# Kernel tuning notes

Measured on AMD Instinct MI355X. Metric: run time of the kernel, lower is better.

## Reference

```python
import jax, jax.numpy as jnp
import numpy as np

# Geometry constants hardcoded in the torch module
B, H, W = 1, 256, 256
A, DC = 64, 1024            # n_views, det_count
NSAMP = 512                  # samples per ray for the line integral
DSRC, DDET, SPACING = 500.0, 500.0, 2.0
NPAD = 2048                  # fft padding (next pow2 >= 2*DC)
FEAT = 32


def _bilinear_image(img, px, py):
    """Bilinear sample img (B,H,W) at centered coords px,py (any shape). Zero outside."""
    b, hh, ww = img.shape
    cx = px + (ww - 1) / 2.0
    cy = py + (hh - 1) / 2.0
    x0 = jnp.floor(cx); y0 = jnp.floor(cy)
    fx = cx - x0; fy = cy - y0
    x0i = x0.astype(jnp.int32); y0i = y0.astype(jnp.int32)
    flat = img.reshape(b, -1)

    def gather(yi, xi):
        valid = (yi >= 0) & (yi < hh) & (xi >= 0) & (xi < ww)
        yc = jnp.clip(yi, 0, hh - 1); xc = jnp.clip(xi, 0, ww - 1)
        idx = (yc * ww + xc).reshape(-1)
        v = jnp.take(flat, idx, axis=1).reshape((b,) + yi.shape)
        return v * valid.astype(img.dtype)

    return (gather(y0i, x0i) * (1 - fx) * (1 - fy)
            + gather(y0i, x0i + 1) * fx * (1 - fy)
            + gather(y0i + 1, x0i) * (1 - fx) * fy
            + gather(y0i + 1, x0i + 1) * fx * fy)


def fan_forward(img, theta):
    """Ray-driven fan-beam forward projection. img (B,1,H,W) -> sino (B,A,DC)."""
    im = img[:, 0]
    c = jnp.cos(theta); s = jnp.sin(theta)
    src = DSRC * jnp.stack([c, s], -1)                    # (A,2) source positions
    e = jnp.stack([-s, c], -1)                            # detector axis
    u = (jnp.arange(DC) - (DC - 1) / 2.0) * SPACING       # detector offsets
    det = -DDET * jnp.stack([c, s], -1)[:, None, :] + u[None, :, None] * e[:, None, :]  # (A,DC,2)
    d = det - src[:, None, :]
    L = jnp.sqrt(jnp.sum(d * d, axis=-1))                 # (A,DC) ray lengths
    t = (jnp.arange(NSAMP, dtype=jnp.float32) + 0.5) / NSAMP
    pts = src[:, None, None, :] + t[None, None, :, None] * d[:, :, None, :]  # (A,DC,N,2)
    vals = _bilinear_image(im, pts[..., 0], pts[..., 1])  # (B,A,DC,N)
    return jnp.sum(vals, axis=-1) * (L / NSAMP)[None]


def filter_sinogram(sino):
    """Ram-Lak ramp filtering along the detector axis with zero-padding."""
    f = jnp.abs(jnp.fft.rfftfreq(NPAD)).astype(jnp.float32)  # cycles/sample
    sf = jnp.fft.rfft(sino, n=NPAD, axis=-1) * (2.0 * f)
    return jnp.fft.irfft(sf, n=NPAD, axis=-1)[..., :DC].astype(sino.dtype)


def fan_backprojection(sino, theta):
    """Pixel-driven fan-beam backprojection. sino (B,A,DC) -> (B,1,H,W)."""
    xs = jnp.arange(W, dtype=jnp.float32) - (W - 1) / 2.0
    ys = jnp.arange(H, dtype=jnp.float32) - (H - 1) / 2.0
    gx, gy = jnp.meshgrid(xs, ys)                         # (H,W)
    c = jnp.cos(theta)[:, None, None]; s = jnp.sin(theta)[:, None, None]
    xr = gx[None] * c + gy[None] * s                      # (A,H,W) rotated coords
    yr = -gx[None] * s + gy[None] * c
    denom = DSRC - xr
    uu = yr * (DSRC + DDET) / denom                       # detector coordinate
    wgt = (DSRC * DSRC) / (denom * denom)                 # fan-beam distance weight
    iu = uu / SPACING + (DC - 1) / 2.0
    i0 = jnp.floor(iu); fr = iu - i0
    i0i = i0.astype(jnp.int32)
    aidx = jnp.arange(A)[:, None, None]
    b = sino.shape[0]
    flat = sino.reshape(b, -1)

    def g(ii):
        valid = (ii >= 0) & (ii < DC)
        ic = jnp.clip(ii, 0, DC - 1)
        idx = (aidx * DC + ic).reshape(-1)
        v = jnp.take(flat, idx, axis=1).reshape((b, A, H, W))
        return v * valid.astype(sino.dtype)

    vals = g(i0i) * (1 - fr) + g(i0i + 1) * fr            # (B,A,H,W)
    bp = jnp.sum(vals * wgt[None], axis=1) * (jnp.pi / A)
    return bp[:, None]


def conv(x, w):
    return jax.lax.conv_general_dilated(x, w, (1, 1), 'SAME',
                                        dimension_numbers=('NCHW', 'OIHW', 'NCHW'))


def setup_inputs():
    key = jax.random.key(0)
    ks = jax.random.split(key, 8)
    x = jax.random.normal(ks[0], (B, 1, H, W), jnp.float32)
    theta = jnp.arange(A, dtype=jnp.float32) * (2.0 * np.pi / A)
    sinogram = jax.random.normal(ks[1], (B, A, DC), jnp.float32)

    def xav(k, shape):
        fan_in = shape[1] * 9; fan_out = shape[0] * 9
        return jax.random.normal(k, shape, jnp.float32) * np.sqrt(2.0 / (fan_in + fan_out)).astype(np.float32)

    return {
        'x': x, 'theta': theta, 'sinogram': sinogram,
        'lambda_step': jnp.float32(0.5), 'soft_thr': jnp.float32(0.01),
        'conv1_forward': xav(ks[2], (FEAT, 1, 3, 3)),
        'conv2_forward': xav(ks[3], (FEAT, FEAT, 3, 3)),
        'conv1_backward': xav(ks[4], (FEAT, FEAT, 3, 3)),
        'conv2_backward': xav(ks[5], (1, FEAT, 3, 3)),
    }


def reference(x, theta, sinogram, lambda_step, soft_thr,
              conv1_forward, conv2_forward, conv1_backward, conv2_backward):
    sino_pred = fan_forward(x, theta)
    filtered = filter_sinogram(sino_pred)
    X_fbp = fan_backprojection(filtered - sinogram, theta)
    x_input = x - lambda_step * X_fbp
    h = jax.nn.relu(conv(x_input, conv1_forward))
    x_forward = conv(h, conv2_forward)
    hs = jnp.sign(x_forward) * jax.nn.relu(jnp.abs(x_forward) - soft_thr)
    x_pred = conv(jax.nn.relu(conv(hs, conv1_backward)), conv2_backward)
    x_est = conv(jax.nn.relu(conv(x_forward, conv1_backward)), conv2_backward)
    symloss = x_est - x_input
    return (x_pred, symloss)
```

## Files before the change

kernel.cpp:

```cpp
#include <hip/hip_runtime.h>

#define DEV_INLINE __device__ __forceinline__

#define PI_F 3.14159265358979323846f

#define H_OFF     0
#define SINO_OFF  2048
#define DIFF_OFF  67584
#define XIN_OFF   133120
#define WF2F_OFF  198656
#define WF1B_OFF  207872
#define WF2B_OFF  212480
#define BUFA_OFF  217088
#define BUFB_OFF  2314240

typedef short bf16x8 __attribute__((ext_vector_type(8)));
typedef float f32x4 __attribute__((ext_vector_type(4)));

union FragI4 { int4 i4; bf16x8 v; };
union FragI  { int i[4]; bf16x8 v; };
union I4U    { int4 i4; int i[4]; };

DEV_INLINE unsigned rne1(float a) {
  unsigned u = __float_as_uint(a);
  return (u + 0x7FFFu + ((u >> 16) & 1u)) >> 16;
}
DEV_INLINE int pack_rne(float a, float b) {
  return (int)(rne1(a) | (rne1(b) << 16));
}

__global__ __launch_bounds__(256) void setup_kernel(
    const float* __restrict__ sino_in, const float* __restrict__ w2f,
    const float* __restrict__ w1b, const float* __restrict__ w2b,
    const float* __restrict__ img,
    float* __restrict__ h, float* __restrict__ diff,
    int* __restrict__ wf2f, int* __restrict__ wf1b, int* __restrict__ wf2b,
    float4* __restrict__ quadP, float* __restrict__ x_input) {
  const int b = blockIdx.x;
  const int tid = threadIdx.x;
  if (b < 64) {
    __shared__ float hp[8][32];
    const int cell = tid & 31;
    const int kq = tid >> 5;
    const int n = b * 32 + cell;
    float ssum = 0.0f;
    const float ang_scale = PI_F / 1024.0f;
    for (int k = kq * 128; k < kq * 128 + 128; ++k) {
      int m = (k * n) & 2047;
      ssum += (float)k * __cosf((float)m * ang_scale);
    }
    hp[kq][cell] = ssum;
    __syncthreads();
    if (tid < 32) {
      float S = 0.0f;
      #pragma unroll
      for (int q = 0; q < 8; ++q) S += hp[q][tid];
      int nn = b * 32 + tid;
      float sgn = (nn & 1) ? -1.0f : 1.0f;
      h[nn] = (S * (1.0f / 512.0f) + sgn) * (1.0f / 2048.0f);
    }
  } else if (b < 320) {
    int idx = (b - 64) * 256 + tid;
    diff[idx] = -sino_in[idx];
  } else if (b < 356) {
    const bool second = (b >= 338);
    int idx = (b - (second ? 338 : 320)) * 256 + tid;
    int d = idx & 3;
    int L = (idx >> 2) & 63;
    int jm = idx >> 8;
    int j = jm >> 1, mt = jm & 1;
    int co = mt * 16 + (L & 15);
    int ci0 = (L >> 4) * 8 + 2 * d;
    const float* w = second ? w1b : w2f;
    int v = pack_rne(w[co * 288 + ci0 * 9 + j], w[co * 288 + (ci0 + 1) * 9 + j]);
    (second ? wf1b : wf2f)[idx] = v;
  } else if (b < 617) {
    int idx = (b - 356) * 256 + tid;
    if (idx < 258 * 258) {
      int y = idx / 258;
      int x = idx - y * 258;
      float4 v;
      int ay = y - 1, bx = x - 1;
      bool y0ok = (ay >= 0 && ay < 256);
      bool y1ok = (ay + 1 >= 0 && ay + 1 < 256);
      bool x0ok = (bx >= 0 && bx < 256);
      bool x1ok = (bx + 1 >= 0 && bx + 1 < 256);
      v.x = (y0ok && x0ok) ? img[(ay << 8) + bx] : 0.0f;
      v.y = (y0ok && x1ok) ? img[(ay << 8) + bx + 1] : 0.0f;
      v.z = (y1ok && x0ok) ? img[((ay + 1) << 8) + bx] : 0.0f;
      v.w = (y1ok && x1ok) ? img[((ay + 1) << 8) + bx + 1] : 0.0f;
      quadP[idx] = v;
    }
  } else if (b < 873) {
    int idx = (b - 617) * 256 + tid;
    x_input[idx] = img[idx];
  } else {
    int d = tid & 3;
    int L = tid >> 2;
    int n = L & 15;
    int k0 = (L >> 4) * 8 + 2 * d;
    float lo = (n < 9) ? w2b[k0 * 9 + n] : 0.0f;
    float hi = (n < 9) ? w2b[(k0 + 1) * 9 + n] : 0.0f;
    wf2b[tid] = pack_rne(lo, hi);
  }
}

__global__ __launch_bounds__(256) void fwdproj(
    const float4* __restrict__ quadP, const float* __restrict__ theta,
    float* __restrict__ sino) {
  __shared__ float part[8][32];
  __shared__ float cs[2];
  const int tid = threadIdx.x;
  const int a = blockIdx.x >> 5;
  const int cell = tid & 31;
  const int chunk = tid >> 5;
  const int d = ((blockIdx.x & 31) << 5) + cell;
  if (tid == 0) {
    float th = theta[a];
    cs[0] = cosf(th);
    cs[1] = sinf(th);
  }
  __syncthreads();
  const float c = cs[0], s = cs[1];
  const float u = ((float)d - 511.5f) * 2.0f;
  const float dxv = -1000.0f * c - u * s;
  const float dyv = -1000.0f * s + u * c;
  const float L = sqrtf(1.0e6f + u * u);
  const float sx = fmaf(500.0f, c, 127.5f);
  const float sy = fmaf(500.0f, s, 127.5f);

  float tlo = 0.0f, thi = 1.0f;
  if (fabsf(dxv) > 1e-6f) {
    float inv = 1.0f / dxv;
    float a0 = (-1.0f - sx) * inv, a1 = (256.0f - sx) * inv;
    tlo = fmaxf(tlo, fminf(a0, a1));
    thi = fminf(thi, fmaxf(a0, a1));
  } else if (sx <= -1.0f || sx >= 256.0f) {
    thi = -1.0f;
  }
  if (fabsf(dyv) > 1e-6f) {
    float inv = 1.0f / dyv;
    float a0 = (-1.0f - sy) * inv, a1 = (256.0f - sy) * inv;
    tlo = fmaxf(tlo, fminf(a0, a1));
    thi = fminf(thi, fmaxf(a0, a1));
  } else if (sy <= -1.0f || sy >= 256.0f) {
    thi = -1.0f;
  }
  int imin = (int)ceilf(tlo * 512.0f - 0.5f) - 1;
  imin = imin < 0 ? 0 : imin;
  int imax = (int)floorf(thi * 512.0f - 0.5f) + 1;
  imax = imax > 511 ? 511 : imax;

  float acc = 0.0f;
  for (int i = imin + chunk; i <= imax; i += 8) {
    float t = ((float)i + 0.5f) * (1.0f / 512.0f);
    float cx = fmaf(t, dxv, sx);
    float cy = fmaf(t, dyv, sy);
    cx = fminf(fmaxf(cx, -1.0f), 256.0f);
    cy = fminf(fmaxf(cy, -1.0f), 256.0f);
    float xf = floorf(cx), yf = floorf(cy);
    float fx = cx - xf, fy = cy - yf;
    int ix = (int)xf + 1;
    int iy = (int)yf + 1;
    float4 q = quadP[iy * 258 + ix];
    float gx = 1.0f - fx, gy = 1.0f - fy;
    acc += gy * (gx * q.x + fx * q.y) + fy * (gx * q.z + fx * q.w);
  }
  part[chunk][cell] = acc;
  __syncthreads();
  if (tid < 32) {
    float r = 0.0f;
    #pragma unroll
    for (int q = 0; q < 8; ++q) r += part[q][tid];
    sino[a * 1024 + ((blockIdx.x & 31) << 5) + tid] = r * (L * (1.0f / 512.0f));
  }
}

__global__ __launch_bounds__(256) void filt(
    const float* __restrict__ sino_pred, const float* __restrict__ h,
    float* __restrict__ diff) {
  __shared__ __align__(16) float srow[256];
  __shared__ __align__(16) float hext[4104];
  const int a = blockIdx.x >> 2;
  const int q = blockIdx.x & 3;
  const int tid = threadIdx.x;
  const int k0base = q * 256;
  srow[tid] = sino_pred[a * 1024 + k0base + tid];
  for (int n = tid; n < 4104; n += 256) hext[n] = h[(n - 2051) & 2047];
  __syncthreads();
  const int dd0 = tid * 4;
  float acc0 = 0.f, acc1 = 0.f, acc2 = 0.f, acc3 = 0.f;
  #pragma unroll 4
  for (int kk = 0; kk < 256; kk += 4) {
    float4 sv = *reinterpret_cast<const float4*>(&srow[kk]);
    int nb = dd0 + 2048 - k0base - kk;
    float4 hA = *reinterpret_cast<const float4*>(&hext[nb]);
    float4 hB = *reinterpret_cast<const float4*>(&hext[nb + 4]);
    acc0 = fmaf(sv.x, hA.w, acc0); acc0 = fmaf(sv.y, hA.z, acc0);
    acc0 = fmaf(sv.z, hA.y, acc0); acc0 = fmaf(sv.w, hA.x, acc0);
    acc1 = fmaf(sv.x, hB.x, acc1); acc1 = fmaf(sv.y, hA.w, acc1);
    acc1 = fmaf(sv.z, hA.z, acc1); acc1 = fmaf(sv.w, hA.y, acc1);
    acc2 = fmaf(sv.x, hB.y, acc2); acc2 = fmaf(sv.y, hB.x, acc2);
    acc2 = fmaf(sv.z, hA.w, acc2); acc2 = fmaf(sv.w, hA.z, acc2);
    acc3 = fmaf(sv.x, hB.z, acc3); acc3 = fmaf(sv.y, hB.y, acc3);
    acc3 = fmaf(sv.z, hB.x, acc3); acc3 = fmaf(sv.w, hA.w, acc3);
  }
  float* o = diff + a * 1024 + dd0;
  atomicAdd(o + 0, acc0);
  atomicAdd(o + 1, acc1);
  atomicAdd(o + 2, acc2);
  atomicAdd(o + 3, acc3);
}

__global__ __launch_bounds__(256) void backproj_part(
    const float* __restrict__ diff, const float* __restrict__ theta,
    const float* __restrict__ lam_p, float* __restrict__ x_input) {
  __shared__ float cst[16], snt[16];
  const int tid = threadIdx.x;
  const int tileb = blockIdx.x & 255;
  const int a0 = (blockIdx.x >> 8) << 4;
  if (tid < 16) {
    float th = theta[a0 + tid];
    cst[tid] = cosf(th);
    snt[tid] = sinf(th);
  }
  __syncthreads();
  const int tX = (tileb & 3) << 6;
  const int tY = (tileb >> 2) << 2;
  const int pxi = tX + (tid & 63);
  const int pyi = tY + (tid >> 6);
  const float gx = (float)pxi - 127.5f;
  const float gy = (float)pyi - 127.5f;
  float acc = 0.0f;
  for (int ai = 0; ai < 16; ++ai) {
    float c = cst[ai], s = snt[ai];
    float xr = gx * c + gy * s;
    float yr = gy * c - gx * s;
    float denom = 500.0f - xr;
    float inv = 1.0f / denom;
    float uu = yr * 1000.0f * inv;
    float wgt = 250000.0f * inv * inv;
    float iu = uu * 0.5f + 511.5f;
    float i0f = floorf(iu);
    float fr = iu - i0f;
    int i0 = (int)i0f;
    int c0 = min(max(i0, 0), 1023);
    int c1 = min(max(i0 + 1, 0), 1023);
    float m0 = (i0 >= 0 && i0 < 1024) ? 1.0f : 0.0f;
    float m1 = (i0 + 1 >= 0 && i0 + 1 < 1024) ? 1.0f : 0.0f;
    const float* row = diff + (a0 + ai) * 1024;
    float v0 = row[c0] * m0;
    float v1 = row[c1] * m1;
    acc += (v0 * (1.0f - fr) + v1 * fr) * wgt;
  }
  int p = (pyi << 8) + pxi;
  atomicAdd(x_input + p, -lam_p[0] * 0.04908738521234052f * acc);
}

__global__ __launch_bounds__(256) void conv12f(
    const float* __restrict__ x_input, const float* __restrict__ w1f,
    const int* __restrict__ wf2f, int* __restrict__ xfp) {
  __shared__ float xin[8][68];
  __shared__ int htile[6732];
  const int tid = threadIdx.x;
  const int lane = tid & 63;
  const int wave = tid >> 6;
  const int tX = (blockIdx.x & 3) << 6;
  const int tY = (blockIdx.x >> 2) << 2;

  FragI4 wf[2][9];
  const int4* wfg = (const int4*)wf2f;
  #pragma unroll
  for (int mt = 0; mt < 2; ++mt)
    #pragma unroll
    for (int j = 0; j < 9; ++j) wf[mt][j].i4 = wfg[(j * 2 + mt) * 64 + lane];

  for (int idx = tid; idx < 544; idx += 256) {
    int sy = idx / 68;
    int sx = idx - sy * 68;
    int gy = tY + sy - 2, gx = tX + sx - 2;
    xin[sy][sx] = (gy >= 0 && gy < 256 && gx >= 0 && gx < 256)
                      ? x_input[(gy << 8) + gx] : 0.0f;
  }
  __syncthreads();

  for (int pos = tid; pos < 396; pos += 256) {
    int yy = pos / 66;
    int xx = pos - yy * 66;
    int hy = tY + yy - 1, hx = tX + xx - 1;
    bool hin = (hy >= 0 && hy < 256 && hx >= 0 && hx < 256);
    float v[9];
    #pragma unroll
    for (int dy = 0; dy < 3; ++dy)
      #pragma unroll
      for (int dx = 0; dx < 3; ++dx) v[dy * 3 + dx] = xin[yy + dy][xx + dx];
    #pragma unroll
    for (int c2 = 0; c2 < 16; ++c2) {
      float r0 = 0.0f, r1 = 0.0f;
      #pragma unroll
      for (int j = 0; j < 9; ++j) {
        r0 = fmaf(v[j], w1f[(2 * c2) * 9 + j], r0);
        r1 = fmaf(v[j], w1f[(2 * c2 + 1) * 9 + j], r1);
      }
      r0 = hin ? fmaxf(r0, 0.0f) : 0.0f;
      r1 = hin ? fmaxf(r1, 0.0f) : 0.0f;
      htile[pos * 17 + c2] = pack_rne(r0, r1);
    }
  }
  __syncthreads();

  const int y = wave;
  const int n = lane & 15;
  const int q = lane >> 4;
  for (int xt = 0; xt < 4; ++xt) {
    const int x0 = xt << 4;
    f32x4 acc0 = {0.f, 0.f, 0.f, 0.f};
    f32x4 acc1 = {0.f, 0.f, 0.f, 0.f};
    #pragma unroll
    for (int j = 0; j < 9; ++j) {
      int dy = j / 3, dx = j - dy * 3;
      int pb = (y + dy) * 66 + x0 + dx;
      int base = (pb + n) * 17 + q * 4;
      FragI bf;
      bf.i[0] = htile[base];
      bf.i[1] = htile[base + 1];
      bf.i[2] = htile[base + 2];
      bf.i[3] = htile[base + 3];
      acc0 = __builtin_amdgcn_mfma_f32_16x16x32_bf16(wf[0][j].v, bf.v, acc0, 0, 0, 0);
      acc1 = __builtin_amdgcn_mfma_f32_16x16x32_bf16(wf[1][j].v, bf.v, acc1, 0, 0, 0);
    }
    const int gpos = ((tY + y) << 8) + tX + x0 + n;
    int2* xp = (int2*)(xfp + (gpos << 4));
    xp[q]     = make_int2(pack_rne(acc0[0], acc0[1]), pack_rne(acc0[2], acc0[3]));
    xp[4 + q] = make_int2(pack_rne(acc1[0], acc1[1]), pack_rne(acc1[2], acc1[3]));
  }
}

__global__ __launch_bounds__(256) void branch_tail(
    const int* __restrict__ xfp, const int* __restrict__ wf1b,
    const int* __restrict__ wf2b, const float* __restrict__ thr_p,
    const float* __restrict__ x_input, float* __restrict__ out) {
  __shared__ int ldsX[9248];
  __shared__ int ldsD[6800];
  float* ldsP = (float*)ldsX;
  const int tid = threadIdx.x;
  const int lane = tid & 63;
  const int wave = tid >> 6;
  const int branch = blockIdx.x >> 8;
  const int tileb = blockIdx.x & 255;
  const int tX = (tileb & 3) << 6;
  const int tY = (tileb >> 2) << 2;
  const float thr = thr_p[0];
  const bool soft = (branch == 0);

  FragI4 wf[2][9];
  const int4* wfg = (const int4*)wf1b;
  #pragma unroll
  for (int mt = 0; mt < 2; ++mt)
    #pragma unroll
    for (int j = 0; j < 9; ++j) wf[mt][j].i4 = wfg[(j * 2 + mt) * 64 + lane];
  FragI4 wb;
  wb.i4 = ((const int4*)wf2b)[lane];

  #pragma unroll
  for (int t = 0; t < 3; ++t) {
    int p = tid + t * 256;
    if (p < 544) {
      int sy = p / 68;
      int sx = p - sy * 68;
      int gy = tY + sy - 2, gx = tX + sx - 2;
      bool ok = ((unsigned)gy < 256u) && ((unsigned)gx < 256u);
      I4U w0, w1, w2, w3;
      if (ok) {
        const int4* src = (const int4*)(xfp + (((gy << 8) + gx) << 4));
        w0.i4 = src[0]; w1.i4 = src[1]; w2.i4 = src[2]; w3.i4 = src[3];
      } else {
        w0.i4 = w1.i4 = w2.i4 = w3.i4 = make_int4(0, 0, 0, 0);
      }
      int base = p * 17;
      #pragma unroll
      for (int k = 0; k < 4; ++k) {
        int vals[4] = {w0.i[k], w1.i[k], w2.i[k], w3.i[k]};
        (void)vals;
      }
      I4U* grp[4] = {&w0, &w1, &w2, &w3};
      #pragma unroll
      for (int g = 0; g < 4; ++g) {
        #pragma unroll
        for (int k = 0; k < 4; ++k) {
          int v = grp[g]->i[k];
          if (soft) {
            float lo = __uint_as_float(((unsigned)v) << 16);
            float hi = __uint_as_float(((unsigned)v) & 0xFFFF0000u);
            lo = fmaxf(lo - thr, 0.0f) + fminf(lo + thr, 0.0f);
            hi = fmaxf(hi - thr, 0.0f) + fminf(hi + thr, 0.0f);
            v = pack_rne(lo, hi);
          }
          ldsX[base + g * 4 + k] = v;
        }
      }
    }
  }
  __syncthreads();

  const int n = lane & 15;
  const int q = lane >> 4;
  const int rxtab[5] = {-1, 15, 31, 47, 49};
  for (int t = wave; t < 30; t += 4) {
    int trow = t / 5;
    int ry = trow - 1;
    int rx0 = rxtab[t - trow * 5];
    int rxn = rx0 + n;
    bool inimg = ((unsigned)(tX + rxn) < 256u) && ((unsigned)(tY + ry) < 256u);
    int wrbase = ((ry + 1) * 66 + rxn + 1) * 17;
    f32x4 acc0 = {0.f, 0.f, 0.f, 0.f};
    f32x4 acc1 = {0.f, 0.f, 0.f, 0.f};
    #pragma unroll
    for (int j = 0; j < 9; ++j) {
      int dy = j / 3, dx = j - dy * 3;
      int pb = (ry + 1 + dy) * 68 + rx0 + 1 + dx;
      int base = (pb + n) * 17 + q * 4;
      FragI bf;
      bf.i[0] = ldsX[base];
      bf.i[1] = ldsX[base + 1];
      bf.i[2] = ldsX[base + 2];
      bf.i[3] = ldsX[base + 3];
      acc0 = __builtin_amdgcn_mfma_f32_16x16x32_bf16(wf[0][j].v, bf.v, acc0, 0, 0, 0);
      acc1 = __builtin_amdgcn_mfma_f32_16x16x32_bf16(wf[1][j].v, bf.v, acc1, 0, 0, 0);
    }
    float a00 = inimg ? fmaxf(acc0[0], 0.0f) : 0.0f;
    float a01 = inimg ? fmaxf(acc0[1], 0.0f) : 0.0f;
    float a02 = inimg ? fmaxf(acc0[2], 0.0f) : 0.0f;
    float a03 = inimg ? fmaxf(acc0[3], 0.0f) : 0.0f;
    float a10 = inimg ? fmaxf(acc1[0], 0.0f) : 0.0f;
    float a11 = inimg ? fmaxf(acc1[1], 0.0f) : 0.0f;
    float a12 = inimg ? fmaxf(acc1[2], 0.0f) : 0.0f;
    float a13 = inimg ? fmaxf(acc1[3], 0.0f) : 0.0f;
    ldsD[wrbase + q * 2]         = pack_rne(a00, a01);
    ldsD[wrbase + q * 2 + 1]     = pack_rne(a02, a03);
    ldsD[wrbase + 8 + q * 2]     = pack_rne(a10, a11);
    ldsD[wrbase + 8 + q * 2 + 1] = pack_rne(a12, a13);
  }
  __syncthreads();

  for (int t = wave; t < 25; t += 4) {
    int pbase = t << 4;
    int abase = (pbase + n) * 17 + q * 4;
    FragI af;
    af.i[0] = ldsD[abase];
    af.i[1] = ldsD[abase + 1];
    af.i[2] = ldsD[abase + 2];
    af.i[3] = ldsD[abase + 3];
    f32x4 acc = {0.f, 0.f, 0.f, 0.f};
    acc = __builtin_amdgcn_mfma_f32_16x16x32_bf16(af.v, wb.v, acc, 0, 0, 0);
    #pragma unroll
    for (int r = 0; r < 4; ++r)
      ldsP[(pbase + q * 4 + r) * 17 + n] = acc[r];
  }
  __syncthreads();

  const int px = tid & 63, py = tid >> 6;
  float acc = 0.0f;
  #pragma unroll
  for (int j = 0; j < 9; ++j) {
    int dy = j / 3, dx = j - dy * 3;
    int rp = (py + dy) * 66 + px + dx;
    acc += ldsP[rp * 17 + j];
  }
  const int p = ((tY + py) << 8) + tX + px;
  if (branch == 0) out[p] = acc;
  else out[65536 + p] = acc - x_input[p];
}

extern "C" void kernel_launch(void* const* d_in, const int* in_sizes, int n_in,
                              void* d_out, int out_size, void* d_ws, size_t ws_size,
                              hipStream_t stream) {
  const float* x       = (const float*)d_in[0];
  const float* theta   = (const float*)d_in[1];
  const float* sino_in = (const float*)d_in[2];
  const float* lam     = (const float*)d_in[3];
  const float* thr     = (const float*)d_in[4];
  const float* w_c1f   = (const float*)d_in[5];
  const float* w_c2f   = (const float*)d_in[6];
  const float* w_c1b   = (const float*)d_in[7];
  const float* w_c2b   = (const float*)d_in[8];
  float* out = (float*)d_out;
  float* ws  = (float*)d_ws;

  float* h         = ws + H_OFF;
  float* sino_pred = ws + SINO_OFF;
  float* diff      = ws + DIFF_OFF;
  float* x_input   = ws + XIN_OFF;
  int*   wf2f      = (int*)(ws + WF2F_OFF);
  int*   wf1b      = (int*)(ws + WF1B_OFF);
  int*   wf2b      = (int*)(ws + WF2B_OFF);
  float4* quadP    = (float4*)(ws + BUFA_OFF);
  int*   xfp       = (int*)(ws + BUFB_OFF);

  setup_kernel<<<874, 256, 0, stream>>>(sino_in, w_c2f, w_c1b, w_c2b, x, h,
                                        diff, wf2f, wf1b, wf2b, quadP, x_input);
  fwdproj<<<2048, 256, 0, stream>>>(quadP, theta, sino_pred);
  filt<<<256, 256, 0, stream>>>(sino_pred, h, diff);
  backproj_part<<<1024, 256, 0, stream>>>(diff, theta, lam, x_input);
  conv12f<<<256, 256, 0, stream>>>(x_input, w_c1f, wf2f, xfp);
  branch_tail<<<512, 256, 0, stream>>>(xfp, wf1b, wf2b, thr, x_input, out);
}
```

Measured before the change: 131.5 us.

## Use channel-group-major LDS layout with 128-bit accesses and halve conv12f tile width

Result: faster. 127.4 us (-3.1%).

```diff
diff --git a/kernel.cpp b/kernel.cpp
--- a/kernel.cpp
+++ b/kernel.cpp
@@ -18,7 +18,6 @@
 typedef float f32x4 __attribute__((ext_vector_type(4)));
 
 union FragI4 { int4 i4; bf16x8 v; };
-union FragI  { int i[4]; bf16x8 v; };
 union I4U    { int4 i4; int i[4]; };
 
 DEV_INLINE unsigned rne1(float a) {
@@ -260,13 +259,13 @@
 __global__ __launch_bounds__(256) void conv12f(
     const float* __restrict__ x_input, const float* __restrict__ w1f,
     const int* __restrict__ wf2f, int* __restrict__ xfp) {
-  __shared__ float xin[8][68];
-  __shared__ int htile[6732];
+  __shared__ float xin[8][36];
+  __shared__ __align__(16) int htile[3264];
   const int tid = threadIdx.x;
   const int lane = tid & 63;
   const int wave = tid >> 6;
-  const int tX = (blockIdx.x & 3) << 6;
-  const int tY = (blockIdx.x >> 2) << 2;
+  const int tX = (blockIdx.x & 7) << 5;
+  const int tY = (blockIdx.x >> 3) << 2;
 
   FragI4 wf[2][9];
   const int4* wfg = (const int4*)wf2f;
@@ -275,18 +274,18 @@
     #pragma unroll
     for (int j = 0; j < 9; ++j) wf[mt][j].i4 = wfg[(j * 2 + mt) * 64 + lane];
 
-  for (int idx = tid; idx < 544; idx += 256) {
-    int sy = idx / 68;
-    int sx = idx - sy * 68;
+  for (int idx = tid; idx < 288; idx += 256) {
+    int sy = idx / 36;
+    int sx = idx - sy * 36;
     int gy = tY + sy - 2, gx = tX + sx - 2;
     xin[sy][sx] = (gy >= 0 && gy < 256 && gx >= 0 && gx < 256)
                       ? x_input[(gy << 8) + gx] : 0.0f;
   }
   __syncthreads();
 
-  for (int pos = tid; pos < 396; pos += 256) {
-    int yy = pos / 66;
-    int xx = pos - yy * 66;
+  for (int pos = tid; pos < 204; pos += 256) {
+    int yy = pos / 34;
+    int xx = pos - yy * 34;
     int hy = tY + yy - 1, hx = tX + xx - 1;
     bool hin = (hy >= 0 && hy < 256 && hx >= 0 && hx < 256);
     float v[9];
@@ -294,6 +293,7 @@
     for (int dy = 0; dy < 3; ++dy)
       #pragma unroll
       for (int dx = 0; dx < 3; ++dx) v[dy * 3 + dx] = xin[yy + dy][xx + dx];
+    int packs[16];
     #pragma unroll
     for (int c2 = 0; c2 < 16; ++c2) {
       float r0 = 0.0f, r1 = 0.0f;
@@ -304,28 +304,30 @@
       }
       r0 = hin ? fmaxf(r0, 0.0f) : 0.0f;
       r1 = hin ? fmaxf(r1, 0.0f) : 0.0f;
-      htile[pos * 17 + c2] = pack_rne(r0, r1);
-    }
+      packs[c2] = pack_rne(r0, r1);
+    }
+    #pragma unroll
+    for (int g = 0; g < 4; ++g)
+      *reinterpret_cast<int4*>(&htile[g * 816 + pos * 4]) =
+          make_int4(packs[4 * g], packs[4 * g + 1],
+                    packs[4 * g + 2], packs[4 * g + 3]);
   }
   __syncthreads();
 
   const int y = wave;
   const int n = lane & 15;
   const int q = lane >> 4;
-  for (int xt = 0; xt < 4; ++xt) {
+  const int qb = q * 816;
+  for (int xt = 0; xt < 2; ++xt) {
     const int x0 = xt << 4;
     f32x4 acc0 = {0.f, 0.f, 0.f, 0.f};
     f32x4 acc1 = {0.f, 0.f, 0.f, 0.f};
     #pragma unroll
     for (int j = 0; j < 9; ++j) {
       int dy = j / 3, dx = j - dy * 3;
-      int pb = (y + dy) * 66 + x0 + dx;
-      int base = (pb + n) * 17 + q * 4;
-      FragI bf;
-      bf.i[0] = htile[base];
-      bf.i[1] = htile[base + 1];
-      bf.i[2] = htile[base + 2];
-      bf.i[3] = htile[base + 3];
+      int pb = (y + dy) * 34 + x0 + dx + n;
+      FragI4 bf;
+      bf.i4 = *reinterpret_cast<const int4*>(&htile[qb + pb * 4]);
       acc0 = __builtin_amdgcn_mfma_f32_16x16x32_bf16(wf[0][j].v, bf.v, acc0, 0, 0, 0);
       acc1 = __builtin_amdgcn_mfma_f32_16x16x32_bf16(wf[1][j].v, bf.v, acc1, 0, 0, 0);
     }
@@ -340,8 +342,8 @@
     const int* __restrict__ xfp, const int* __restrict__ wf1b,
     const int* __restrict__ wf2b, const float* __restrict__ thr_p,
     const float* __restrict__ x_input, float* __restrict__ out) {
-  __shared__ int ldsX[9248];
-  __shared__ int ldsD[6800];
+  __shared__ __align__(16) int ldsX[8704];
+  __shared__ __align__(16) int ldsD[6400];
   float* ldsP = (float*)ldsX;
   const int tid = threadIdx.x;
   const int lane = tid & 63;
@@ -362,6 +364,11 @@
   FragI4 wb;
   wb.i4 = ((const int4*)wf2b)[lane];
 
+  if (tid < 16) {
+    int g = tid >> 2, px = 396 + (tid & 3);
+    *reinterpret_cast<int4*>(&ldsD[g * 1600 + px * 4]) = make_int4(0, 0, 0, 0);
+  }
+
   #pragma unroll
   for (int t = 0; t < 3; ++t) {
     int p = tid + t * 256;
@@ -370,34 +377,27 @@
       int sx = p - sy * 68;
       int gy = tY + sy - 2, gx = tX + sx - 2;
       bool ok = ((unsigned)gy < 256u) && ((unsigned)gx < 256u);
-      I4U w0, w1, w2, w3;
+      I4U w[4];
       if (ok) {
         const int4* src = (const int4*)(xfp + (((gy << 8) + gx) << 4));
-        w0.i4 = src[0]; w1.i4 = src[1]; w2.i4 = src[2]; w3.i4 = src[3];
+        w[0].i4 = src[0]; w[1].i4 = src[1]; w[2].i4 = src[2]; w[3].i4 = src[3];
       } else {
-        w0.i4 = w1.i4 = w2.i4 = w3.i4 = make_int4(0, 0, 0, 0);
+        w[0].i4 = w[1].i4 = w[2].i4 = w[3].i4 = make_int4(0, 0, 0, 0);
       }
-      int base = p * 17;
-      #pragma unroll
-      for (int k = 0; k < 4; ++k) {
-        int vals[4] = {w0.i[k], w1.i[k], w2.i[k], w3.i[k]};
-        (void)vals;
-      }
-      I4U* grp[4] = {&w0, &w1, &w2, &w3};
       #pragma unroll
       for (int g = 0; g < 4; ++g) {
-        #pragma unroll
-        for (int k = 0; k < 4; ++k) {
-          int v = grp[g]->i[k];
-          if (soft) {
+        if (soft) {
+          #pragma unroll
+          for (int k = 0; k < 4; ++k) {
+            int v = w[g].i[k];
             float lo = __uint_as_float(((unsigned)v) << 16);
             float hi = __uint_as_float(((unsigned)v) & 0xFFFF0000u);
             lo = fmaxf(lo - thr, 0.0f) + fminf(lo + thr, 0.0f);
             hi = fmaxf(hi - thr, 0.0f) + fminf(hi + thr, 0.0f);
-            v = pack_rne(lo, hi);
+            w[g].i[k] = pack_rne(lo, hi);
           }
-          ldsX[base + g * 4 + k] = v;
         }
+        *reinterpret_cast<int4*>(&ldsX[g * 2176 + p * 4]) = w[g].i4;
       }
     }
   }
@@ -412,19 +412,15 @@
     int rx0 = rxtab[t - trow * 5];
     int rxn = rx0 + n;
     bool inimg = ((unsigned)(tX + rxn) < 256u) && ((unsigned)(tY + ry) < 256u);
-    int wrbase = ((ry + 1) * 66 + rxn + 1) * 17;
+    int pxD = (ry + 1) * 66 + rxn + 1;
     f32x4 acc0 = {0.f, 0.f, 0.f, 0.f};
     f32x4 acc1 = {0.f, 0.f, 0.f, 0.f};
     #pragma unroll
     for (int j = 0; j < 9; ++j) {
       int dy = j / 3, dx = j - dy * 3;
-      int pb = (ry + 1 + dy) * 68 + rx0 + 1 + dx;
-      int base = (pb + n) * 17 + q * 4;
-      FragI bf;
-      bf.i[0] = ldsX[base];
-      bf.i[1] = ldsX[base + 1];
-      bf.i[2] = ldsX[base + 2];
-      bf.i[3] = ldsX[base + 3];
+      int pb = (ry + 1 + dy) * 68 + rx0 + 1 + dx + n;
+      FragI4 bf;
+      bf.i4 = *reinterpret_cast<const int4*>(&ldsX[q * 2176 + pb * 4]);
       acc0 = __builtin_amdgcn_mfma_f32_16x16x32_bf16(wf[0][j].v, bf.v, acc0, 0, 0, 0);
       acc1 = __builtin_amdgcn_mfma_f32_16x16x32_bf16(wf[1][j].v, bf.v, acc1, 0, 0, 0);
     }
@@ -436,21 +432,19 @@
     float a11 = inimg ? fmaxf(acc1[1], 0.0f) : 0.0f;
     float a12 = inimg ? fmaxf(acc1[2], 0.0f) : 0.0f;
     float a13 = inimg ? fmaxf(acc1[3], 0.0f) : 0.0f;
-    ldsD[wrbase + q * 2]         = pack_rne(a00, a01);
-    ldsD[wrbase + q * 2 + 1]     = pack_rne(a02, a03);
-    ldsD[wrbase + 8 + q * 2]     = pack_rne(a10, a11);
-    ldsD[wrbase + 8 + q * 2 + 1] = pack_rne(a12, a13);
+    *reinterpret_cast<int2*>(
+        &ldsD[(q >> 1) * 1600 + pxD * 4 + (q & 1) * 2]) =
+        make_int2(pack_rne(a00, a01), pack_rne(a02, a03));
+    *reinterpret_cast<int2*>(
+        &ldsD[(2 + (q >> 1)) * 1600 + pxD * 4 + (q & 1) * 2]) =
+        make_int2(pack_rne(a10, a11), pack_rne(a12, a13));
   }
   __syncthreads();
 
   for (int t = wave; t < 25; t += 4) {
     int pbase = t << 4;
-    int abase = (pbase + n) * 17 + q * 4;
-    FragI af;
-    af.i[0] = ldsD[abase];
-    af.i[1] = ldsD[abase + 1];
-    af.i[2] = ldsD[abase + 2];
-    af.i[3] = ldsD[abase + 3];
+    FragI4 af;
+    af.i4 = *reinterpret_cast<const int4*>(&ldsD[q * 1600 + (pbase + n) * 4]);
     f32x4 acc = {0.f, 0.f, 0.f, 0.f};
     acc = __builtin_amdgcn_mfma_f32_16x16x32_bf16(af.v, wb.v, acc, 0, 0, 0);
     #pragma unroll
@@ -502,6 +496,6 @@
   fwdproj<<<2048, 256, 0, stream>>>(quadP, theta, sino_pred);
   filt<<<256, 256, 0, stream>>>(sino_pred, h, diff);
   backproj_part<<<1024, 256, 0, stream>>>(diff, theta, lam, x_input);
-  conv12f<<<256, 256, 0, stream>>>(x_input, w_c1f, wf2f, xfp);
+  conv12f<<<512, 256, 0, stream>>>(x_input, w_c1f, wf2f, xfp);
   branch_tail<<<512, 256, 0, stream>>>(xfp, wf1b, wf2b, thr, x_input, out);
 }
```
